# Kernel optimization log

Measured on AMD Instinct MI355X. Metric: run time of the kernel, lower is better.

Reference implementation:

```python
import jax, jax.numpy as jnp
import numpy as np

# module hyperparameters (from init_kwargs)
STEP = 16
LEAK = 32
KS = STEP + LEAK          # temporal kernel size = padding = fodep = 48
STRIDE = 2
FODEP = KS
WINNERS = 0.5             # fraction used for winner_fodep cap
C_IN, C_OUT, K = 2, 64, 3
DENSE = 0.3
THETA = DENSE * K * K * C_IN   # 5.4
BIAS0 = 0.5
W_INIT = DENSE


def setup_inputs() -> dict:
    key = jax.random.key(0)
    k1, k2 = jax.random.split(key)
    # input spike train [B, C_in, H, W, T]
    input_spikes = jax.random.uniform(k1, (4, C_IN, 48, 48, 96), jnp.float32)
    # Exponential(rate=1/w_init) sample clipped to [0,1], like the torch init
    u = jax.random.uniform(k2, (C_OUT, C_IN, K, K), jnp.float32, 1e-7, 1.0)
    weight = jnp.clip(-W_INIT * jnp.log(u), 0.0, 1.0)
    bias = jnp.full((C_OUT,), BIAS0, jnp.float32)
    return {"input_spikes": input_spikes, "weight": weight, "bias": bias}


def _step_fire_leak(weight):
    # StepFireLeakKernel.forward: max(0, min(t/step, -(t - w*step)/leak + w)), flipped in time
    t = jnp.arange(KS, dtype=weight.dtype)          # [KS]
    w = weight[..., None]                           # [O,I,K,K,1]
    kern = jnp.maximum(0.0, jnp.minimum(t / STEP, -(t - w * STEP) / LEAK + w))
    return kern[..., ::-1]                          # [O,I,K,K,KS]


def _potentials(input_spikes, weight, bias):
    x = jnp.transpose(input_spikes, (0, 1, 4, 2, 3))              # [B,C,T,H,W]
    wk = jnp.transpose(_step_fire_leak(weight), (0, 1, 4, 2, 3))  # [O,I,KS,K,K]
    p = jax.lax.conv_general_dilated(
        x, wk,
        window_strides=(1, STRIDE, STRIDE),
        padding=((KS, KS), (0, 0), (0, 0)),
        dimension_numbers=("NCDHW", "OIDHW", "NCDHW"))
    p = p + bias[None, :, None, None, None]
    return jnp.transpose(p, (0, 1, 3, 4, 2))                      # [B,O,X,Y,T']


def _winner_takes_all(potentials):
    B, C, X, Y, T = potentials.shape
    N = X * Y
    pot = jnp.transpose(potentials.reshape(B, C, N, T), (3, 0, 2, 1))  # [T,B,N,C]
    winner_cap = int(np.ceil(WINNERS * N))

    def step(depression, p_t):
        # depression: [B,N] int32 refractory counters
        active = (depression == 0).astype(p_t.dtype)[..., None]                      # [B,N,1]
        k_ok = ((depression != 0).sum(-1) < winner_cap).astype(p_t.dtype)[:, None, None]
        p = p_t * active * k_ok                                                      # [B,N,C]
        winner = jnp.argmax(p, axis=-1)                                              # [B,N]
        spike = (jnp.max(p, axis=-1) > THETA).astype(jnp.int32)                      # [B,N]
        winners_t = jax.nn.one_hot(winner, C, dtype=jnp.int32) * spike[..., None]    # scatter at winner
        depression = jnp.clip(depression + spike * FODEP - 1, 0, FODEP - 1)
        return depression, winners_t

    dep0 = jnp.zeros((B, N), jnp.int32)
    _, winners = jax.lax.scan(step, dep0, pot)                    # winners: [T,B,N,C]
    out = jnp.transpose(winners, (1, 3, 2, 0)).reshape(B, C, X, Y, T)
    return out.astype(jnp.float32)


def reference(input_spikes, weight, bias):
    potentials = _potentials(input_spikes, weight, bias)
    return _winner_takes_all(potentials)
```

## Files before the change

kernel.cpp:

```cpp
#include <hip/hip_runtime.h>

#define B_    4
#define CI_   2
#define H_    48
#define W_    48
#define T_    96
#define CO_   64
#define XO_   23
#define NSITE 529
#define TP_   145
#define TPAD_ 200
#define NTAP_ 18
#define THETA_ 5.4f
#define FODEP_ 48
#define WCAP_  265
#define NOUT4 (19636480 / 4)

#define WS_WKF 0
#define WS_KS  55296
#define WS_M   (55296 + 1152)
#define WS_A   (WS_M + 306820)

__global__ void k_wk(const float* __restrict__ weight, float* __restrict__ wkf,
                     int* __restrict__ kstab) {
    int idx = blockIdx.x * 256 + threadIdx.x;
    if (idx >= CO_ * NTAP_) return;
    int o = idx / NTAP_, tap = idx % NTAP_;
    int i = tap / 9, kx = (tap % 9) / 3, ky = tap % 3;
    float w = weight[((o * CI_ + i) * 3 + kx) * 3 + ky];
    int ktlo = 48;
    for (int kt = 0; kt < 48; ++kt) {
        float j = (float)(47 - kt);
        float v = fmaxf(0.0f, fminf(j * (1.0f / 16.0f), 1.5f * w - j * (1.0f / 32.0f)));
        wkf[idx * 48 + kt] = v;
        if (v > 0.0f && ktlo == 48) ktlo = kt;
    }
    kstab[idx] = (ktlo >= 48) ? 48 : (ktlo - ktlo % 5);
}

#define SEGP(S) \
    { float k0 = wrow[(S)],   k1 = wrow[(S)+1], k2 = wrow[(S)+2], \
            k3 = wrow[(S)+3], k4 = wrow[(S)+4]; \
      float n0 = sptr[(S)+10], n1 = sptr[(S)+11], n2 = sptr[(S)+12], \
            n3 = sptr[(S)+13], n4 = sptr[(S)+14]; \
      a0 = fmaf(k0, w0, a0); a1 = fmaf(k0, w1, a1); a2 = fmaf(k0, w2, a2); \
      a3 = fmaf(k0, w3, a3); a4 = fmaf(k0, w4, a4); \
      a0 = fmaf(k1, w1, a0); a1 = fmaf(k1, w2, a1); a2 = fmaf(k1, w3, a2); \
      a3 = fmaf(k1, w4, a3); a4 = fmaf(k1, w5, a4); \
      a0 = fmaf(k2, w2, a0); a1 = fmaf(k2, w3, a1); a2 = fmaf(k2, w4, a2); \
      a3 = fmaf(k2, w5, a3); a4 = fmaf(k2, w6, a4); \
      a0 = fmaf(k3, w3, a0); a1 = fmaf(k3, w4, a1); a2 = fmaf(k3, w5, a2); \
      a3 = fmaf(k3, w6, a3); a4 = fmaf(k3, w7, a4); \
      a0 = fmaf(k4, w4, a0); a1 = fmaf(k4, w5, a1); a2 = fmaf(k4, w6, a2); \
      a3 = fmaf(k4, w7, a3); a4 = fmaf(k4, w8, a4); \
      w0 = w5; w1 = w6; w2 = w7; w3 = w8; w4 = w9; \
      w5 = n0; w6 = n1; w7 = n2; w8 = n3; w9 = n4; }

__launch_bounds__(512, 8)
__global__ void k_conv(const float* __restrict__ in, const float* __restrict__ wkf,
                       const int* __restrict__ kstab, const float* __restrict__ bias,
                       float* __restrict__ m_out, int* __restrict__ a_out,
                       float4* __restrict__ out4) {
    __shared__ __align__(16) union {
        float sp[30][TPAD_];
        struct { float m[8][64][5]; int a[8][64][5]; } red;
    } u;

    int bid = blockIdx.x;
    int b  = bid / (XO_ * 12);
    int r  = bid % (XO_ * 12);
    int x  = r / 12;
    int y0 = (r % 12) * 2;
    int tid  = threadIdx.x;
    int lane = tid & 63;
    int dy   = lane >> 5;
    int tg   = lane & 31;
    int t0   = (tg < 29) ? tg * 5 : 140;
    int y    = y0 + dy;
    bool valid = (y < XO_) && (tg < 29);

    {
        int stride = gridDim.x * blockDim.x;
        float4 z = make_float4(0.f, 0.f, 0.f, 0.f);
        for (int i2 = bid * blockDim.x + tid; i2 < NOUT4; i2 += stride) out4[i2] = z;
    }

    for (int q = tid; q < 30 * TPAD_ / 4; q += 512)
        ((float4*)u.sp)[q] = make_float4(0.f, 0.f, 0.f, 0.f);
    __syncthreads();
    for (int q = tid; q < 30 * 24; q += 512) {
        int row = q / 24, f4 = q % 24;
        int c = row % 5, rr = row / 5;
        int kx = rr % 3, i = rr / 3;
        int col = 2 * y0 + c;
        if (col < W_) {
            const float4* src = (const float4*)(in +
                ((((size_t)b * CI_ + i) * H_ + (2 * x + kx)) * W_ + col) * T_);
            *(float4*)(&u.sp[row][48 + f4 * 4]) = src[f4];
        }
    }
    __syncthreads();

    float mbest[5];
    int   abest[5];
#pragma unroll
    for (int j = 0; j < 5; ++j) { mbest[j] = -1e30f; abest[j] = 0; }

    int wq    = __builtin_amdgcn_readfirstlane(tid >> 6);
    int obase = wq * 8;
    const float* sbase = &u.sp[0][0] + 2 * dy * TPAD_ + t0;

#pragma unroll 1
    for (int oi = 0; oi < 8; ++oi) {
        int o = obase + oi;
        const int* ksrow = kstab + o * NTAP_;
        const float* wrow = wkf + o * (NTAP_ * 48);
        const float* sptr = sbase;
        int ky3 = 0;
        float a0 = 0.f, a1 = 0.f, a2 = 0.f, a3 = 0.f, a4 = 0.f;
        int ks_next = ksrow[0];
#pragma unroll 1
        for (int tap = 0; tap < NTAP_; ++tap) {
            int ks = __builtin_amdgcn_readfirstlane(ks_next);
            if (tap + 1 < NTAP_) ks_next = ksrow[tap + 1];
            if (ks < 48) {
                const float* sk = sptr + ks;
                float w0 = sk[0], w1 = sk[1], w2 = sk[2], w3 = sk[3], w4 = sk[4],
                      w5 = sk[5], w6 = sk[6], w7 = sk[7], w8 = sk[8], w9 = sk[9];
                if (ks <= 0)  SEGP(0)
                if (ks <= 5)  SEGP(5)
                if (ks <= 10) SEGP(10)
                if (ks <= 15) SEGP(15)
                if (ks <= 20) SEGP(20)
                if (ks <= 25) SEGP(25)
                if (ks <= 30) SEGP(30)
                if (ks <= 35) SEGP(35)
                if (ks <= 40) SEGP(40)
                {
                    float k45 = wrow[45], k46 = wrow[46];
                    a0 = fmaf(k45, w0, a0); a1 = fmaf(k45, w1, a1); a2 = fmaf(k45, w2, a2);
                    a3 = fmaf(k45, w3, a3); a4 = fmaf(k45, w4, a4);
                    a0 = fmaf(k46, w1, a0); a1 = fmaf(k46, w2, a1); a2 = fmaf(k46, w3, a2);
                    a3 = fmaf(k46, w4, a3); a4 = fmaf(k46, w5, a4);
                }
            }
            wrow += 48;
            if (++ky3 == 3) { ky3 = 0; sptr += 3 * TPAD_; }
            else            { sptr += TPAD_; }
        }
        float bo = bias[o];
        float p0 = a0 + bo, p1 = a1 + bo, p2 = a2 + bo, p3 = a3 + bo, p4 = a4 + bo;
        if (p0 > mbest[0]) { mbest[0] = p0; abest[0] = o; }
        if (p1 > mbest[1]) { mbest[1] = p1; abest[1] = o; }
        if (p2 > mbest[2]) { mbest[2] = p2; abest[2] = o; }
        if (p3 > mbest[3]) { mbest[3] = p3; abest[3] = o; }
        if (p4 > mbest[4]) { mbest[4] = p4; abest[4] = o; }
    }

    __syncthreads();
#pragma unroll
    for (int j = 0; j < 5; ++j) { u.red.m[wq][lane][j] = mbest[j]; u.red.a[wq][lane][j] = abest[j]; }
    __syncthreads();
    if (wq == 0 && valid) {
        int site = x * XO_ + y;
#pragma unroll
        for (int j = 0; j < 5; ++j) {
            float mv = u.red.m[0][lane][j];
            int   av = u.red.a[0][lane][j];
#pragma unroll
            for (int w = 1; w < 8; ++w) {
                float m2 = u.red.m[w][lane][j];
                if (m2 > mv) { mv = m2; av = u.red.a[w][lane][j]; }
            }
            size_t off = ((size_t)b * TP_ + (t0 + j)) * NSITE + site;
            m_out[off] = mv;
            a_out[off] = av;
        }
    }
}

__launch_bounds__(576)
__global__ void k_wta(const float* __restrict__ m_in, const int* __restrict__ a_in,
                      float* __restrict__ out) {
    int b = blockIdx.x;
    int tid = threadIdx.x;
    int lane = tid & 63;
    int wid = tid >> 6;
    __shared__ int cnts[2][9];

    bool site = (tid < NSITE);
    const float* mb = m_in + (size_t)b * TP_ * NSITE;
    const int*   ab = a_in + (size_t)b * TP_ * NSITE;
    int dep = 0;
    float mv = site ? mb[tid] : 0.f;
    int   av = site ? ab[tid] : 0;

    for (int t = 0; t < TP_; ++t) {
        unsigned long long ball = __ballot(dep != 0);
        if (lane == 0) cnts[t & 1][wid] = __popcll(ball);
        float mv2 = 0.f; int av2 = 0;
        if (site && t + 1 < TP_) {
            mv2 = mb[(t + 1) * NSITE + tid];
            av2 = ab[(t + 1) * NSITE + tid];
        }
        __syncthreads();
        int tot = 0;
#pragma unroll
        for (int w = 0; w < 9; ++w) tot += cnts[t & 1][w];
        if (site) {
            if ((tot < WCAP_) && (dep == 0) && (mv > THETA_)) {
                out[(((size_t)b * CO_ + av) * NSITE + tid) * TP_ + t] = 1.0f;
                dep = FODEP_ - 1;
            } else {
                dep = dep ? dep - 1 : 0;
            }
        }
        mv = mv2; av = av2;
    }
}

extern "C" void kernel_launch(void* const* d_in, const int* in_sizes, int n_in,
                              void* d_out, int out_size, void* d_ws, size_t ws_size,
                              hipStream_t stream) {
    const float* in     = (const float*)d_in[0];
    const float* weight = (const float*)d_in[1];
    const float* bias   = (const float*)d_in[2];
    float* out = (float*)d_out;

    float* wkf   = (float*)d_ws + WS_WKF;
    int*   kstab = (int*)((float*)d_ws + WS_KS);
    float* m     = (float*)d_ws + WS_M;
    int*   a     = (int*)((float*)d_ws + WS_A);

    k_wk<<<(CO_ * NTAP_ + 255) / 256, 256, 0, stream>>>(weight, wkf, kstab);
    k_conv<<<B_ * XO_ * 12, 512, 0, stream>>>(in, wkf, kstab, bias, m, a, (float4*)out);
    k_wta<<<B_, 576, 0, stream>>>(m, a, out);
}
```

Baseline: 408.5 us.

## Use persistent grid for conv and ping-pong registers to drop shift moves

The conv kernel now runs on a fixed grid of 1024 blocks that loop over the 1104 work items, instead of one block per item. The sliding-window register shift (ten moves per segment) is replaced by alternating A/B segment macros that reload into whichever register half has been consumed. A parity bit packed into kstab selects the starting register assignment. This is meant to cut VALU move instructions and spread the output zero-fill differently, but some blocks now process two items serially, which creates a tail imbalance.

```diff
diff --git a/kernel.cpp b/kernel.cpp
--- a/kernel.cpp
+++ b/kernel.cpp
@@ -11,6 +11,8 @@
 #define TP_   145
 #define TPAD_ 200
 #define NTAP_ 18
+#define NITEM (B_ * XO_ * 12)
+#define GRID_ 1024
 #define THETA_ 5.4f
 #define FODEP_ 48
 #define WCAP_  265
@@ -35,26 +37,52 @@
         wkf[idx * 48 + kt] = v;
         if (v > 0.0f && ktlo == 48) ktlo = kt;
     }
-    kstab[idx] = (ktlo >= 48) ? 48 : (ktlo - ktlo % 5);
-}
-
-#define SEGP(S) \
-    { float k0 = wrow[(S)],   k1 = wrow[(S)+1], k2 = wrow[(S)+2], \
+    if (ktlo >= 48) { kstab[idx] = 48; return; }
+    int ks = ktlo - ktlo % 5;
+    kstab[idx] = ks | (((ks / 5) & 1) << 8);
+}
+
+#define SEGA(S) \
+    { float k0 = wrow[(S)], k1 = wrow[(S)+1], k2 = wrow[(S)+2], \
             k3 = wrow[(S)+3], k4 = wrow[(S)+4]; \
-      float n0 = sptr[(S)+10], n1 = sptr[(S)+11], n2 = sptr[(S)+12], \
-            n3 = sptr[(S)+13], n4 = sptr[(S)+14]; \
-      a0 = fmaf(k0, w0, a0); a1 = fmaf(k0, w1, a1); a2 = fmaf(k0, w2, a2); \
-      a3 = fmaf(k0, w3, a3); a4 = fmaf(k0, w4, a4); \
-      a0 = fmaf(k1, w1, a0); a1 = fmaf(k1, w2, a1); a2 = fmaf(k1, w3, a2); \
-      a3 = fmaf(k1, w4, a3); a4 = fmaf(k1, w5, a4); \
-      a0 = fmaf(k2, w2, a0); a1 = fmaf(k2, w3, a1); a2 = fmaf(k2, w4, a2); \
-      a3 = fmaf(k2, w5, a3); a4 = fmaf(k2, w6, a4); \
-      a0 = fmaf(k3, w3, a0); a1 = fmaf(k3, w4, a1); a2 = fmaf(k3, w5, a2); \
-      a3 = fmaf(k3, w6, a3); a4 = fmaf(k3, w7, a4); \
-      a0 = fmaf(k4, w4, a0); a1 = fmaf(k4, w5, a1); a2 = fmaf(k4, w6, a2); \
-      a3 = fmaf(k4, w7, a3); a4 = fmaf(k4, w8, a4); \
-      w0 = w5; w1 = w6; w2 = w7; w3 = w8; w4 = w9; \
-      w5 = n0; w6 = n1; w7 = n2; w8 = n3; w9 = n4; }
+      a0 = fmaf(k0, c0, a0); a1 = fmaf(k0, c1, a1); a2 = fmaf(k0, c2, a2); \
+      a3 = fmaf(k0, c3, a3); a4 = fmaf(k0, c4, a4); c0 = sptr[(S)+10]; \
+      a0 = fmaf(k1, c1, a0); a1 = fmaf(k1, c2, a1); a2 = fmaf(k1, c3, a2); \
+      a3 = fmaf(k1, c4, a3); a4 = fmaf(k1, n0, a4); c1 = sptr[(S)+11]; \
+      a0 = fmaf(k2, c2, a0); a1 = fmaf(k2, c3, a1); a2 = fmaf(k2, c4, a2); \
+      a3 = fmaf(k2, n0, a3); a4 = fmaf(k2, n1, a4); c2 = sptr[(S)+12]; \
+      a0 = fmaf(k3, c3, a0); a1 = fmaf(k3, c4, a1); a2 = fmaf(k3, n0, a2); \
+      a3 = fmaf(k3, n1, a3); a4 = fmaf(k3, n2, a4); c3 = sptr[(S)+13]; \
+      a0 = fmaf(k4, c4, a0); a1 = fmaf(k4, n0, a1); a2 = fmaf(k4, n1, a2); \
+      a3 = fmaf(k4, n2, a3); a4 = fmaf(k4, n3, a4); c4 = sptr[(S)+14]; }
+
+#define SEGB(S) \
+    { float k0 = wrow[(S)], k1 = wrow[(S)+1], k2 = wrow[(S)+2], \
+            k3 = wrow[(S)+3], k4 = wrow[(S)+4]; \
+      a0 = fmaf(k0, n0, a0); a1 = fmaf(k0, n1, a1); a2 = fmaf(k0, n2, a2); \
+      a3 = fmaf(k0, n3, a3); a4 = fmaf(k0, n4, a4); n0 = sptr[(S)+10]; \
+      a0 = fmaf(k1, n1, a0); a1 = fmaf(k1, n2, a1); a2 = fmaf(k1, n3, a2); \
+      a3 = fmaf(k1, n4, a3); a4 = fmaf(k1, c0, a4); n1 = sptr[(S)+11]; \
+      a0 = fmaf(k2, n2, a0); a1 = fmaf(k2, n3, a1); a2 = fmaf(k2, n4, a2); \
+      a3 = fmaf(k2, c0, a3); a4 = fmaf(k2, c1, a4); n2 = sptr[(S)+12]; \
+      a0 = fmaf(k3, n3, a0); a1 = fmaf(k3, n4, a1); a2 = fmaf(k3, c0, a2); \
+      a3 = fmaf(k3, c1, a3); a4 = fmaf(k3, c2, a4); n3 = sptr[(S)+13]; \
+      a0 = fmaf(k4, n4, a0); a1 = fmaf(k4, c0, a1); a2 = fmaf(k4, c1, a2); \
+      a3 = fmaf(k4, c2, a3); a4 = fmaf(k4, c3, a4); n4 = sptr[(S)+14]; }
+
+#define SEGAL(S) \
+    { float k0 = wrow[(S)], k1 = wrow[(S)+1], k2 = wrow[(S)+2], \
+            k3 = wrow[(S)+3], k4 = wrow[(S)+4]; \
+      a0 = fmaf(k0, c0, a0); a1 = fmaf(k0, c1, a1); a2 = fmaf(k0, c2, a2); \
+      a3 = fmaf(k0, c3, a3); a4 = fmaf(k0, c4, a4); c0 = sptr[(S)+10]; \
+      a0 = fmaf(k1, c1, a0); a1 = fmaf(k1, c2, a1); a2 = fmaf(k1, c3, a2); \
+      a3 = fmaf(k1, c4, a3); a4 = fmaf(k1, n0, a4); \
+      a0 = fmaf(k2, c2, a0); a1 = fmaf(k2, c3, a1); a2 = fmaf(k2, c4, a2); \
+      a3 = fmaf(k2, n0, a3); a4 = fmaf(k2, n1, a4); \
+      a0 = fmaf(k3, c3, a0); a1 = fmaf(k3, c4, a1); a2 = fmaf(k3, n0, a2); \
+      a3 = fmaf(k3, n1, a3); a4 = fmaf(k3, n2, a4); \
+      a0 = fmaf(k4, c4, a0); a1 = fmaf(k4, n0, a1); a2 = fmaf(k4, n1, a2); \
+      a3 = fmaf(k4, n2, a3); a4 = fmaf(k4, n3, a4); }
 
 __launch_bounds__(512, 8)
 __global__ void k_conv(const float* __restrict__ in, const float* __restrict__ wkf,
@@ -67,115 +95,132 @@
     } u;
 
     int bid = blockIdx.x;
-    int b  = bid / (XO_ * 12);
-    int r  = bid % (XO_ * 12);
-    int x  = r / 12;
-    int y0 = (r % 12) * 2;
     int tid  = threadIdx.x;
     int lane = tid & 63;
     int dy   = lane >> 5;
     int tg   = lane & 31;
     int t0   = (tg < 29) ? tg * 5 : 140;
-    int y    = y0 + dy;
-    bool valid = (y < XO_) && (tg < 29);
-
-    {
-        int stride = gridDim.x * blockDim.x;
-        float4 z = make_float4(0.f, 0.f, 0.f, 0.f);
-        for (int i2 = bid * blockDim.x + tid; i2 < NOUT4; i2 += stride) out4[i2] = z;
-    }
-
-    for (int q = tid; q < 30 * TPAD_ / 4; q += 512)
-        ((float4*)u.sp)[q] = make_float4(0.f, 0.f, 0.f, 0.f);
-    __syncthreads();
-    for (int q = tid; q < 30 * 24; q += 512) {
-        int row = q / 24, f4 = q % 24;
-        int c = row % 5, rr = row / 5;
-        int kx = rr % 3, i = rr / 3;
-        int col = 2 * y0 + c;
-        if (col < W_) {
-            const float4* src = (const float4*)(in +
-                ((((size_t)b * CI_ + i) * H_ + (2 * x + kx)) * W_ + col) * T_);
-            *(float4*)(&u.sp[row][48 + f4 * 4]) = src[f4];
-        }
-    }
-    __syncthreads();
-
-    float mbest[5];
-    int   abest[5];
-#pragma unroll
-    for (int j = 0; j < 5; ++j) { mbest[j] = -1e30f; abest[j] = 0; }
-
     int wq    = __builtin_amdgcn_readfirstlane(tid >> 6);
     int obase = wq * 8;
-    const float* sbase = &u.sp[0][0] + 2 * dy * TPAD_ + t0;
+
+    {
+        float4 z = make_float4(0.f, 0.f, 0.f, 0.f);
+        for (int i2 = bid * 512 + tid; i2 < NOUT4; i2 += GRID_ * 512) out4[i2] = z;
+    }
 
 #pragma unroll 1
-    for (int oi = 0; oi < 8; ++oi) {
-        int o = obase + oi;
-        const int* ksrow = kstab + o * NTAP_;
-        const float* wrow = wkf + o * (NTAP_ * 48);
-        const float* sptr = sbase;
-        int ky3 = 0;
-        float a0 = 0.f, a1 = 0.f, a2 = 0.f, a3 = 0.f, a4 = 0.f;
-        int ks_next = ksrow[0];
+    for (int item = bid; item < NITEM; item += GRID_) {
+        int b  = item / (XO_ * 12);
+        int r  = item % (XO_ * 12);
+        int x  = r / 12;
+        int y0 = (r % 12) * 2;
+        int y  = y0 + dy;
+        bool valid = (y < XO_) && (tg < 29);
+
+        for (int q = tid; q < 30 * TPAD_ / 4; q += 512)
+            ((float4*)u.sp)[q] = make_float4(0.f, 0.f, 0.f, 0.f);
+        __syncthreads();
+        for (int q = tid; q < 30 * 24; q += 512) {
+            int row = q / 24, f4 = q % 24;
+            int c = row % 5, rr = row / 5;
+            int kx = rr % 3, i = rr / 3;
+            int col = 2 * y0 + c;
+            if (col < W_) {
+                const float4* src = (const float4*)(in +
+                    ((((size_t)b * CI_ + i) * H_ + (2 * x + kx)) * W_ + col) * T_);
+                *(float4*)(&u.sp[row][48 + f4 * 4]) = src[f4];
+            }
+        }
+        __syncthreads();
+
+        float mbest[5];
+        int   abest[5];
+#pragma unroll
+        for (int j = 0; j < 5; ++j) { mbest[j] = -1e30f; abest[j] = 0; }
+
+        const float* sbase = &u.sp[0][0] + 2 * dy * TPAD_ + t0;
+
 #pragma unroll 1
-        for (int tap = 0; tap < NTAP_; ++tap) {
-            int ks = __builtin_amdgcn_readfirstlane(ks_next);
-            if (tap + 1 < NTAP_) ks_next = ksrow[tap + 1];
-            if (ks < 48) {
-                const float* sk = sptr + ks;
-                float w0 = sk[0], w1 = sk[1], w2 = sk[2], w3 = sk[3], w4 = sk[4],
-                      w5 = sk[5], w6 = sk[6], w7 = sk[7], w8 = sk[8], w9 = sk[9];
-                if (ks <= 0)  SEGP(0)
-                if (ks <= 5)  SEGP(5)
-                if (ks <= 10) SEGP(10)
-                if (ks <= 15) SEGP(15)
-                if (ks <= 20) SEGP(20)
-                if (ks <= 25) SEGP(25)
-                if (ks <= 30) SEGP(30)
-                if (ks <= 35) SEGP(35)
-                if (ks <= 40) SEGP(40)
-                {
-                    float k45 = wrow[45], k46 = wrow[46];
-                    a0 = fmaf(k45, w0, a0); a1 = fmaf(k45, w1, a1); a2 = fmaf(k45, w2, a2);
-                    a3 = fmaf(k45, w3, a3); a4 = fmaf(k45, w4, a4);
-                    a0 = fmaf(k46, w1, a0); a1 = fmaf(k46, w2, a1); a2 = fmaf(k46, w3, a2);
-                    a3 = fmaf(k46, w4, a3); a4 = fmaf(k46, w5, a4);
+        for (int oi = 0; oi < 8; ++oi) {
+            int o = obase + oi;
+            const int* ksrow = kstab + o * NTAP_;
+            const float* wrow = wkf + o * (NTAP_ * 48);
+            const float* sptr = sbase;
+            int ky3 = 0;
+            float a0 = 0.f, a1 = 0.f, a2 = 0.f, a3 = 0.f, a4 = 0.f;
+            int ks_next = ksrow[0];
+#pragma unroll 1
+            for (int tap = 0; tap < NTAP_; ++tap) {
+                int ksv = __builtin_amdgcn_readfirstlane(ks_next);
+                if (tap + 1 < NTAP_) ks_next = ksrow[tap + 1];
+                int ks = ksv & 63;
+                if (ks < 48) {
+                    int par = ksv >> 8;
+                    const float* sk = sptr + ks;
+                    float c0, c1, c2, c3, c4, n0, n1, n2, n3, n4;
+                    if (par == 0) {
+                        c0 = sk[0]; c1 = sk[1]; c2 = sk[2]; c3 = sk[3]; c4 = sk[4];
+                        n0 = sk[5]; n1 = sk[6]; n2 = sk[7]; n3 = sk[8]; n4 = sk[9];
+                    } else {
+                        n0 = sk[0]; n1 = sk[1]; n2 = sk[2]; n3 = sk[3]; n4 = sk[4];
+                        c0 = sk[5]; c1 = sk[6]; c2 = sk[7]; c3 = sk[8]; c4 = sk[9];
+                    }
+                    if (ks <= 0)  SEGA(0)
+                    if (ks <= 5)  SEGB(5)
+                    if (ks <= 10) SEGA(10)
+                    if (ks <= 15) SEGB(15)
+                    if (ks <= 20) SEGA(20)
+                    if (ks <= 25) SEGB(25)
+                    if (ks <= 30) SEGA(30)
+                    if (ks <= 35) SEGB(35)
+                    if (ks <= 40) SEGAL(40)
+                    {
+                        float k45 = wrow[45], k46 = wrow[46];
+                        a0 = fmaf(k45, n0, a0); a1 = fmaf(k45, n1, a1);
+                        a2 = fmaf(k45, n2, a2); a3 = fmaf(k45, n3, a3);
+                        a4 = fmaf(k45, n4, a4);
+                        a0 = fmaf(k46, n1, a0); a1 = fmaf(k46, n2, a1);
+                        a2 = fmaf(k46, n3, a2); a3 = fmaf(k46, n4, a3);
+                        a4 = fmaf(k46, c0, a4);
+                    }
                 }
-            }
-            wrow += 48;
-            if (++ky3 == 3) { ky3 = 0; sptr += 3 * TPAD_; }
-            else            { sptr += TPAD_; }
-        }
-        float bo = bias[o];
-        float p0 = a0 + bo, p1 = a1 + bo, p2 = a2 + bo, p3 = a3 + bo, p4 = a4 + bo;
-        if (p0 > mbest[0]) { mbest[0] = p0; abest[0] = o; }
-        if (p1 > mbest[1]) { mbest[1] = p1; abest[1] = o; }
-        if (p2 > mbest[2]) { mbest[2] = p2; abest[2] = o; }
-        if (p3 > mbest[3]) { mbest[3] = p3; abest[3] = o; }
-        if (p4 > mbest[4]) { mbest[4] = p4; abest[4] = o; }
-    }
-
-    __syncthreads();
-#pragma unroll
-    for (int j = 0; j < 5; ++j) { u.red.m[wq][lane][j] = mbest[j]; u.red.a[wq][lane][j] = abest[j]; }
-    __syncthreads();
-    if (wq == 0 && valid) {
-        int site = x * XO_ + y;
+                wrow += 48;
+                if (++ky3 == 3) { ky3 = 0; sptr += 3 * TPAD_; }
+                else            { sptr += TPAD_; }
+            }
+            float bo = bias[o];
+            float p0 = a0 + bo, p1 = a1 + bo, p2 = a2 + bo, p3 = a3 + bo, p4 = a4 + bo;
+            if (p0 > mbest[0]) { mbest[0] = p0; abest[0] = o; }
+            if (p1 > mbest[1]) { mbest[1] = p1; abest[1] = o; }
+            if (p2 > mbest[2]) { mbest[2] = p2; abest[2] = o; }
+            if (p3 > mbest[3]) { mbest[3] = p3; abest[3] = o; }
+            if (p4 > mbest[4]) { mbest[4] = p4; abest[4] = o; }
+        }
+
+        __syncthreads();
 #pragma unroll
         for (int j = 0; j < 5; ++j) {
-            float mv = u.red.m[0][lane][j];
-            int   av = u.red.a[0][lane][j];
-#pragma unroll
-            for (int w = 1; w < 8; ++w) {
-                float m2 = u.red.m[w][lane][j];
-                if (m2 > mv) { mv = m2; av = u.red.a[w][lane][j]; }
-            }
-            size_t off = ((size_t)b * TP_ + (t0 + j)) * NSITE + site;
-            m_out[off] = mv;
-            a_out[off] = av;
-        }
+            u.red.m[wq][lane][j] = mbest[j];
+            u.red.a[wq][lane][j] = abest[j];
+        }
+        __syncthreads();
+        if (wq == 0 && valid) {
+            int site = x * XO_ + y;
+#pragma unroll
+            for (int j = 0; j < 5; ++j) {
+                float mv = u.red.m[0][lane][j];
+                int   av = u.red.a[0][lane][j];
+#pragma unroll
+                for (int w = 1; w < 8; ++w) {
+                    float m2 = u.red.m[w][lane][j];
+                    if (m2 > mv) { mv = m2; av = u.red.a[w][lane][j]; }
+                }
+                size_t off = ((size_t)b * TP_ + (t0 + j)) * NSITE + site;
+                m_out[off] = mv;
+                a_out[off] = av;
+            }
+        }
+        __syncthreads();
     }
 }
 
@@ -233,6 +278,6 @@
     int*   a     = (int*)((float*)d_ws + WS_A);
 
     k_wk<<<(CO_ * NTAP_ + 255) / 256, 256, 0, stream>>>(weight, wkf, kstab);
-    k_conv<<<B_ * XO_ * 12, 512, 0, stream>>>(in, wkf, kstab, bias, m, a, (float4*)out);
+    k_conv<<<GRID_, 512, 0, stream>>>(in, wkf, kstab, bias, m, a, (float4*)out);
     k_wta<<<B_, 576, 0, stream>>>(m, a, out);
 }
```

Measured after the change: 368.7 us. 1.11x faster.
